# Optimization experiments

Hardware: AMD Instinct MI355X
Metric: run time of the kernel (lower is better)

## Reference

```python
import jax, jax.numpy as jnp
import numpy as np

IN_F = 4096
OUT_F = 4096
RANK = 16
TOKENS = 8192
WORDS = IN_F // 16  # 16 int2 codes per int32 word
LORA_SCALE = 1.0


def pack_int2(codes):
    """codes: [out_f, in_f] int32 in {0,1,2} -> packed [out_f, in_f//16] int32.
    Little-endian: code k of a word sits at bits [2k, 2k+1]."""
    c = codes.reshape(codes.shape[0], -1, 16)  # [out, words, 16]
    shifts = jnp.arange(16, dtype=jnp.int32) * 2
    return jnp.sum(c << shifts, axis=-1).astype(jnp.int32)


def unpack_int2(packed, in_features):
    """packed: [out_f, words] int32 -> ternary floats [out_f, in_f] in {-1,0,+1}."""
    shifts = jnp.arange(16, dtype=jnp.int32) * 2
    codes = (packed[:, :, None] >> shifts) & 3  # [out, words, 16]
    codes = codes.reshape(packed.shape[0], -1)[:, :in_features]
    return codes - 1  # {0,1,2} -> {-1,0,+1}


def setup_inputs() -> dict:
    key = jax.random.key(0)
    kx, kc, ka, km, kb, kA, kB = jax.random.split(key, 7)
    x = jax.random.normal(kx, (TOKENS, IN_F), dtype=jnp.float32)
    codes = jax.random.randint(kc, (OUT_F, IN_F), 0, 3, dtype=jnp.int32)  # {0,1,2}
    int2_packed = pack_int2(codes)  # [OUT_F, WORDS]
    alpha = jax.random.uniform(ka, (OUT_F,), dtype=jnp.float32) * 0.1 + 0.01
    mu = jax.random.normal(km, (OUT_F,), dtype=jnp.float32) * 0.01
    bias = jax.random.normal(kb, (OUT_F,), dtype=jnp.float32) * 0.02
    lora_A = jax.random.normal(kA, (RANK, IN_F), dtype=jnp.float32) * 0.02
    lora_B = jax.random.normal(kB, (OUT_F, RANK), dtype=jnp.float32) * 0.02
    return {"x": x, "int2_packed": int2_packed, "alpha": alpha, "mu": mu,
            "bias": bias, "lora_A": lora_A, "lora_B": lora_B}


def reference(x, int2_packed, alpha, mu, bias, lora_A, lora_B):
    # Unpack ternary weight T in {-1,0,+1}: [OUT_F, IN_F]
    T = unpack_int2(int2_packed, IN_F).astype(x.dtype)
    # ternary matmul, per-row scale alpha
    out = jnp.einsum('ti,oi->to', x, T) * alpha[None, :]
    # asymmetric shift: mu_o * sum_i x_i
    out = out + mu[None, :] * jnp.sum(x, axis=-1, keepdims=True)
    # LoRA correction: scale * (x A^T) B^T
    lora_out = jnp.einsum('tr,or->to', jnp.einsum('ti,ri->tr', x, lora_A), lora_B)
    out = out + LORA_SCALE * lora_out
    return out + bias[None, :]
```

## Files before the change

kernel.cpp:

```cpp
#include <hip/hip_runtime.h>
#include <stdint.h>

#define IN_F   4096
#define OUT_F  4096
#define TOKENS 8192
#define RANK   16

#define BM 128
#define BN 128
#define BKI 64

typedef unsigned short u16;
typedef __attribute__((ext_vector_type(8))) short bf16x8;
typedef __attribute__((ext_vector_type(4))) float f32x4;
typedef __attribute__((ext_vector_type(4))) int i32x4;

#define GLDS16(g, l) __builtin_amdgcn_global_load_lds( \
    (__attribute__((address_space(1))) void*)(g),      \
    (__attribute__((address_space(3))) void*)(l), 16, 0, 0)

__device__ __forceinline__ u16 bf16bits(float f) {
    unsigned int u = __builtin_bit_cast(unsigned int, f);
    unsigned int lsb = (u >> 16) & 1u;
    u += 0x7fffu + lsb;
    return (u16)(u >> 16);
}

__device__ __forceinline__ unsigned int quant4(float a, float b, float c, float d, float inv) {
    int qa = __float2int_rn(a * inv); qa = max(-127, min(127, qa));
    int qb = __float2int_rn(b * inv); qb = max(-127, min(127, qb));
    int qc = __float2int_rn(c * inv); qc = max(-127, min(127, qc));
    int qd = __float2int_rn(d * inv); qd = max(-127, min(127, qd));
    return (qa & 255) | ((qb & 255) << 8) | ((qc & 255) << 16) | ((qd & 255) << 24);
}

__global__ __launch_bounds__(256) void k_quant(const float* __restrict__ X,
                                               signed char* __restrict__ Xq,
                                               float* __restrict__ sArr,
                                               float* __restrict__ SArr) {
    const int t = blockIdx.x;
    const int tid = threadIdx.x;
    const int lane = tid & 63;
    const int wv = tid >> 6;

    const float4* X4 = (const float4*)(X + (size_t)t * IN_F);
    float4 v[4];
#pragma unroll
    for (int j = 0; j < 4; j++) v[j] = X4[tid * 4 + j];

    float s = 0.f, m = 0.f;
#pragma unroll
    for (int j = 0; j < 4; j++) {
        s += v[j].x + v[j].y + v[j].z + v[j].w;
        m = fmaxf(m, fmaxf(fmaxf(fabsf(v[j].x), fabsf(v[j].y)),
                           fmaxf(fabsf(v[j].z), fabsf(v[j].w))));
    }
#pragma unroll
    for (int off = 32; off > 0; off >>= 1) {
        s += __shfl_down(s, off);
        m = fmaxf(m, __shfl_down(m, off));
    }
    __shared__ float rs[4], rm[4];
    if (lane == 0) { rs[wv] = s; rm[wv] = m; }
    __syncthreads();
    float S = rs[0] + rs[1] + rs[2] + rs[3];
    float M = fmaxf(fmaxf(rm[0], rm[1]), fmaxf(rm[2], rm[3]));
    M = fmaxf(M, 1e-20f);
    if (tid == 0) { SArr[t] = S; sArr[t] = M / 127.0f; }

    float inv = 127.0f / M;
    uint4 o;
    o.x = quant4(v[0].x, v[0].y, v[0].z, v[0].w, inv);
    o.y = quant4(v[1].x, v[1].y, v[1].z, v[1].w, inv);
    o.z = quant4(v[2].x, v[2].y, v[2].z, v[2].w, inv);
    o.w = quant4(v[3].x, v[3].y, v[3].z, v[3].w, inv);
    *(uint4*)(Xq + (size_t)t * IN_F + tid * 16) = o;
}

__global__ __launch_bounds__(256) void k_aq(const float* __restrict__ lA,
                                            signed char* __restrict__ Aq,
                                            float* __restrict__ aScale) {
    const int r = blockIdx.x;
    const int tid = threadIdx.x;
    const int lane = tid & 63;
    const int wv = tid >> 6;

    const float4* A4 = (const float4*)(lA + (size_t)r * IN_F);
    float4 v[4];
#pragma unroll
    for (int j = 0; j < 4; j++) v[j] = A4[tid * 4 + j];

    float m = 0.f;
#pragma unroll
    for (int j = 0; j < 4; j++)
        m = fmaxf(m, fmaxf(fmaxf(fabsf(v[j].x), fabsf(v[j].y)),
                           fmaxf(fabsf(v[j].z), fabsf(v[j].w))));
#pragma unroll
    for (int off = 32; off > 0; off >>= 1) m = fmaxf(m, __shfl_down(m, off));
    __shared__ float rm[4];
    if (lane == 0) rm[wv] = m;
    __syncthreads();
    float M = fmaxf(fmaxf(rm[0], rm[1]), fmaxf(rm[2], rm[3]));
    M = fmaxf(M, 1e-20f);
    if (tid == 0) aScale[r] = M / 127.0f;

    float inv = 127.0f / M;
    uint4 o;
    o.x = quant4(v[0].x, v[0].y, v[0].z, v[0].w, inv);
    o.y = quant4(v[1].x, v[1].y, v[1].z, v[1].w, inv);
    o.z = quant4(v[2].x, v[2].y, v[2].z, v[2].w, inv);
    o.w = quant4(v[3].x, v[3].y, v[3].z, v[3].w, inv);
    *(uint4*)(Aq + (size_t)r * IN_F + tid * 16) = o;
}

__global__ __launch_bounds__(64) void k_lora_y(const signed char* __restrict__ Xq,
                                               const signed char* __restrict__ Aq,
                                               const float* __restrict__ sArr,
                                               const float* __restrict__ aScale,
                                               u16* __restrict__ ypad) {
    const int lane = threadIdx.x;
    const int t0 = blockIdx.x * 16;
    const int fr = lane & 15;
    const int q16 = (lane >> 4) * 16;

    i32x4 acc = {};
    const signed char* xrow = Xq + (size_t)(t0 + fr) * IN_F + q16;
    const signed char* arow = Aq + (size_t)fr * IN_F + q16;
#pragma unroll 8
    for (int k0 = 0; k0 < IN_F; k0 += BKI) {
        i32x4 af = *(const i32x4*)(xrow + k0);
        i32x4 bf = *(const i32x4*)(arow + k0);
        acc = __builtin_amdgcn_mfma_i32_16x16x64_i8(af, bf, acc, 0, 0, 0);
    }

    const int c0 = lane & 15;
    const int r0 = (lane >> 4) * 4;
    float asc = aScale[c0];
#pragma unroll
    for (int r = 0; r < 4; r++) {
        int t = t0 + r0 + r;
        float y = sArr[t] * asc * (float)acc[r];
        ypad[(size_t)t * 32 + c0] = bf16bits(y);
        ypad[(size_t)t * 32 + 16 + c0] = 0;
    }
}

__global__ __launch_bounds__(256) void k_build_wi8(const int* __restrict__ packed,
                                                   signed char* __restrict__ Wq) {
    int idx = blockIdx.x * 256 + threadIdx.x;
    int p = packed[idx];
    uint4 o;
    unsigned int w[4];
#pragma unroll
    for (int g = 0; g < 4; g++) {
        unsigned int word = 0;
#pragma unroll
        for (int j = 0; j < 4; j++) {
            int k = g * 4 + j;
            int b = ((p >> (2 * k)) & 3) - 1;
            word |= (unsigned int)(b & 255) << (8 * j);
        }
        w[g] = word;
    }
    o.x = w[0]; o.y = w[1]; o.z = w[2]; o.w = w[3];
    *(uint4*)(Wq + (size_t)idx * 16) = o;
}

__global__ __launch_bounds__(256) void k_bl(const float* __restrict__ lB,
                                            u16* __restrict__ Bl) {
    int o = blockIdx.x * 256 + threadIdx.x;
    const float4* B4 = (const float4*)(lB + (size_t)o * RANK);
    float4 b0 = B4[0], b1 = B4[1], b2 = B4[2], b3 = B4[3];
    union { u16 u[32]; uint4 q[4]; } ob;
    ob.u[0] = bf16bits(b0.x); ob.u[1] = bf16bits(b0.y); ob.u[2] = bf16bits(b0.z); ob.u[3] = bf16bits(b0.w);
    ob.u[4] = bf16bits(b1.x); ob.u[5] = bf16bits(b1.y); ob.u[6] = bf16bits(b1.z); ob.u[7] = bf16bits(b1.w);
    ob.u[8] = bf16bits(b2.x); ob.u[9] = bf16bits(b2.y); ob.u[10] = bf16bits(b2.z); ob.u[11] = bf16bits(b2.w);
    ob.u[12] = bf16bits(b3.x); ob.u[13] = bf16bits(b3.y); ob.u[14] = bf16bits(b3.z); ob.u[15] = bf16bits(b3.w);
#pragma unroll
    for (int k = 16; k < 32; k++) ob.u[k] = 0;
    uint4* dst = (uint4*)(Bl + (size_t)o * 32);
    dst[0] = ob.q[0]; dst[1] = ob.q[1]; dst[2] = ob.q[2]; dst[3] = ob.q[3];
}

__global__ __launch_bounds__(256, 2) void k_gemm_i8(const signed char* __restrict__ Xq,
                                                    const signed char* __restrict__ Wq,
                                                    const float* __restrict__ sArr,
                                                    const float* __restrict__ SArr,
                                                    const float* __restrict__ alpha,
                                                    const float* __restrict__ mu,
                                                    const float* __restrict__ bias,
                                                    const u16* __restrict__ ypad,
                                                    const u16* __restrict__ Bl,
                                                    float* __restrict__ out) {
    __shared__ unsigned char smem[16384];
    unsigned char* smA = smem;
    unsigned char* smB = smem + 8192;

    const int tid = threadIdx.x;
    const int lane = tid & 63;
    const int wv = tid >> 6;
    const int wm = (wv >> 1) * 64;
    const int wn = (wv & 1) * 64;
    const int fr = lane & 15;
    const int q16 = (lane >> 4) * 16;
    const int wvbase = wv * 1024;

    const int m0 = blockIdx.y * BM;
    const int n0 = blockIdx.x * BN;

    i32x4 acc[4][4] = {};

    for (int k0 = 0; k0 < IN_F; k0 += BKI) {
        __syncthreads();
#pragma unroll
        for (int i = 0; i < 2; i++) {
            int c = i * 256 + tid;
            int row = c >> 2, off = (c & 3) << 4;
            GLDS16(Xq + (size_t)(m0 + row) * IN_F + k0 + off, smA + i * 4096 + wvbase);
        }
#pragma unroll
        for (int i = 0; i < 2; i++) {
            int c = i * 256 + tid;
            int row = c >> 2, off = (c & 3) << 4;
            GLDS16(Wq + (size_t)(n0 + row) * IN_F + k0 + off, smB + i * 4096 + wvbase);
        }
        __syncthreads();

        i32x4 af[4], bf[4];
#pragma unroll
        for (int mt = 0; mt < 4; mt++)
            af[mt] = *(const i32x4*)(smA + (wm + mt * 16 + fr) * BKI + q16);
#pragma unroll
        for (int nt = 0; nt < 4; nt++)
            bf[nt] = *(const i32x4*)(smB + (wn + nt * 16 + fr) * BKI + q16);
#pragma unroll
        for (int mt = 0; mt < 4; mt++)
#pragma unroll
            for (int nt = 0; nt < 4; nt++)
                acc[mt][nt] = __builtin_amdgcn_mfma_i32_16x16x64_i8(af[mt], bf[nt], acc[mt][nt], 0, 0, 0);
    }

    const int r0 = (lane >> 4) * 4;
    const int c0 = lane & 15;
    f32x4 facc[4][4];
#pragma unroll
    for (int mt = 0; mt < 4; mt++) {
        int rb = m0 + wm + mt * 16 + r0;
        f32x4 sv = *(const f32x4*)(sArr + rb);
        f32x4 Sv = *(const f32x4*)(SArr + rb);
#pragma unroll
        for (int nt = 0; nt < 4; nt++) {
            int col = n0 + wn + nt * 16 + c0;
            float av = alpha[col], mv = mu[col], bv = bias[col];
#pragma unroll
            for (int r = 0; r < 4; r++)
                facc[mt][nt][r] = av * sv[r] * (float)acc[mt][nt][r] + fmaf(mv, Sv[r], bv);
        }
    }

    __syncthreads();
#pragma unroll
    for (int i = 0; i < 2; i++) {
        int c = i * 256 + tid;
        int row = c >> 2, off = (c & 3) << 4;
        GLDS16((const unsigned char*)ypad + (size_t)(m0 + row) * 64 + off, smA + i * 4096 + wvbase);
        GLDS16((const unsigned char*)Bl + (size_t)(n0 + row) * 64 + off, smB + i * 4096 + wvbase);
    }
    __syncthreads();
    bf16x8 yf[4], blf[4];
#pragma unroll
    for (int mt = 0; mt < 4; mt++)
        yf[mt] = *(const bf16x8*)(smA + (wm + mt * 16 + fr) * 64 + q16);
#pragma unroll
    for (int nt = 0; nt < 4; nt++)
        blf[nt] = *(const bf16x8*)(smB + (wn + nt * 16 + fr) * 64 + q16);
#pragma unroll
    for (int mt = 0; mt < 4; mt++)
#pragma unroll
        for (int nt = 0; nt < 4; nt++)
            facc[mt][nt] = __builtin_amdgcn_mfma_f32_16x16x32_bf16(yf[mt], blf[nt], facc[mt][nt], 0, 0, 0);

#pragma unroll
    for (int nt = 0; nt < 4; nt++) {
        int col = n0 + wn + nt * 16 + c0;
#pragma unroll
        for (int mt = 0; mt < 4; mt++) {
            int row = m0 + wm + mt * 16 + r0;
            float* op = out + (size_t)row * OUT_F + col;
#pragma unroll
            for (int r = 0; r < 4; r++)
                op[(size_t)r * OUT_F] = facc[mt][nt][r];
        }
    }
}

extern "C" void kernel_launch(void* const* d_in, const int* in_sizes, int n_in,
                              void* d_out, int out_size, void* d_ws, size_t ws_size,
                              hipStream_t stream) {
    const float* x      = (const float*)d_in[0];
    const int*   packed = (const int*)d_in[1];
    const float* alpha  = (const float*)d_in[2];
    const float* mu     = (const float*)d_in[3];
    const float* bias   = (const float*)d_in[4];
    const float* lA     = (const float*)d_in[5];
    const float* lB     = (const float*)d_in[6];
    float* out = (float*)d_out;

    char* p = (char*)d_ws;
    signed char* Wq = (signed char*)p;             p += (size_t)OUT_F * IN_F;
    signed char* Xq = (signed char*)p;             p += (size_t)TOKENS * IN_F;
    float* sArr = (float*)p;                       p += (size_t)TOKENS * 4;
    float* SArr = (float*)p;                       p += (size_t)TOKENS * 4;
    u16* ypad = (u16*)p;                           p += (size_t)TOKENS * 32 * 2;
    u16* Bl = (u16*)p;                             p += (size_t)OUT_F * 32 * 2;
    signed char* Aq = (signed char*)p;             p += (size_t)RANK * IN_F;
    float* aScale = (float*)p;                     p += RANK * 4;

    k_quant<<<dim3(TOKENS), dim3(256), 0, stream>>>(x, Xq, sArr, SArr);
    k_aq<<<dim3(RANK), dim3(256), 0, stream>>>(lA, Aq, aScale);
    k_lora_y<<<dim3(TOKENS / 16), dim3(64), 0, stream>>>(Xq, Aq, sArr, aScale, ypad);
    k_build_wi8<<<dim3(OUT_F * 256 / 256), dim3(256), 0, stream>>>(packed, Wq);
    k_bl<<<dim3(OUT_F / 256), dim3(256), 0, stream>>>(lB, Bl);

    dim3 grid(OUT_F / BN, TOKENS / BM);
    k_gemm_i8<<<grid, dim3(256), 0, stream>>>(Xq, Wq, sArr, SArr, alpha, mu, bias, ypad, Bl, out);
}
```

Measured before the change: 411.1 us.

## Fuse prep kernels, split-K LoRA projection, and swizzle GEMM LDS tiles

Merges the activation quantization, weight unpacking, LoRA-A quantization and LoRA-B conversion into one launch that dispatches on block index. The LoRA down-projection now uses four waves per block, each covering a quarter of K, with an LDS reduction. The main int8 GEMM XOR-swizzles the 16-byte chunks within each LDS row to cut bank conflicts on the fragment reads. This trades fewer launches and better LDS access for extra index arithmetic and block-type branching.

```diff
diff --git a/kernel.cpp b/kernel.cpp
--- a/kernel.cpp
+++ b/kernel.cpp
@@ -18,6 +18,10 @@
 #define GLDS16(g, l) __builtin_amdgcn_global_load_lds( \
     (__attribute__((address_space(1))) void*)(g),      \
     (__attribute__((address_space(3))) void*)(l), 16, 0, 0)
+
+__device__ __forceinline__ int swz_row(int row) {
+    return (row & 3) ^ ((row >> 2) & 1);
+}
 
 __device__ __forceinline__ u16 bf16bits(float f) {
     unsigned int u = __builtin_bit_cast(unsigned int, f);
@@ -34,152 +38,154 @@
     return (qa & 255) | ((qb & 255) << 8) | ((qc & 255) << 16) | ((qd & 255) << 24);
 }
 
-__global__ __launch_bounds__(256) void k_quant(const float* __restrict__ X,
-                                               signed char* __restrict__ Xq,
-                                               float* __restrict__ sArr,
-                                               float* __restrict__ SArr) {
-    const int t = blockIdx.x;
+__global__ __launch_bounds__(256) void k_prep(const float* __restrict__ X,
+                                              const int* __restrict__ packed,
+                                              const float* __restrict__ lA,
+                                              const float* __restrict__ lB,
+                                              signed char* __restrict__ Xq,
+                                              float* __restrict__ sArr,
+                                              float* __restrict__ SArr,
+                                              signed char* __restrict__ Wq,
+                                              u16* __restrict__ Bl,
+                                              signed char* __restrict__ Aq,
+                                              float* __restrict__ aScale) {
+    __shared__ float rs[4], rm[4];
+    const int b = blockIdx.x;
     const int tid = threadIdx.x;
     const int lane = tid & 63;
     const int wv = tid >> 6;
 
-    const float4* X4 = (const float4*)(X + (size_t)t * IN_F);
-    float4 v[4];
-#pragma unroll
-    for (int j = 0; j < 4; j++) v[j] = X4[tid * 4 + j];
-
-    float s = 0.f, m = 0.f;
-#pragma unroll
-    for (int j = 0; j < 4; j++) {
-        s += v[j].x + v[j].y + v[j].z + v[j].w;
-        m = fmaxf(m, fmaxf(fmaxf(fabsf(v[j].x), fabsf(v[j].y)),
-                           fmaxf(fabsf(v[j].z), fabsf(v[j].w))));
-    }
-#pragma unroll
-    for (int off = 32; off > 0; off >>= 1) {
-        s += __shfl_down(s, off);
-        m = fmaxf(m, __shfl_down(m, off));
-    }
-    __shared__ float rs[4], rm[4];
-    if (lane == 0) { rs[wv] = s; rm[wv] = m; }
-    __syncthreads();
-    float S = rs[0] + rs[1] + rs[2] + rs[3];
-    float M = fmaxf(fmaxf(rm[0], rm[1]), fmaxf(rm[2], rm[3]));
-    M = fmaxf(M, 1e-20f);
-    if (tid == 0) { SArr[t] = S; sArr[t] = M / 127.0f; }
-
-    float inv = 127.0f / M;
-    uint4 o;
-    o.x = quant4(v[0].x, v[0].y, v[0].z, v[0].w, inv);
-    o.y = quant4(v[1].x, v[1].y, v[1].z, v[1].w, inv);
-    o.z = quant4(v[2].x, v[2].y, v[2].z, v[2].w, inv);
-    o.w = quant4(v[3].x, v[3].y, v[3].z, v[3].w, inv);
-    *(uint4*)(Xq + (size_t)t * IN_F + tid * 16) = o;
-}
-
-__global__ __launch_bounds__(256) void k_aq(const float* __restrict__ lA,
-                                            signed char* __restrict__ Aq,
-                                            float* __restrict__ aScale) {
-    const int r = blockIdx.x;
+    if (b < TOKENS) {
+        const int t = b;
+        const float4* X4 = (const float4*)(X + (size_t)t * IN_F);
+        float4 v[4];
+#pragma unroll
+        for (int j = 0; j < 4; j++) v[j] = X4[tid * 4 + j];
+
+        float s = 0.f, m = 0.f;
+#pragma unroll
+        for (int j = 0; j < 4; j++) {
+            s += v[j].x + v[j].y + v[j].z + v[j].w;
+            m = fmaxf(m, fmaxf(fmaxf(fabsf(v[j].x), fabsf(v[j].y)),
+                               fmaxf(fabsf(v[j].z), fabsf(v[j].w))));
+        }
+#pragma unroll
+        for (int off = 32; off > 0; off >>= 1) {
+            s += __shfl_down(s, off);
+            m = fmaxf(m, __shfl_down(m, off));
+        }
+        if (lane == 0) { rs[wv] = s; rm[wv] = m; }
+        __syncthreads();
+        float S = rs[0] + rs[1] + rs[2] + rs[3];
+        float M = fmaxf(fmaxf(rm[0], rm[1]), fmaxf(rm[2], rm[3]));
+        M = fmaxf(M, 1e-20f);
+        if (tid == 0) { SArr[t] = S; sArr[t] = M / 127.0f; }
+
+        float inv = 127.0f / M;
+        uint4 o;
+        o.x = quant4(v[0].x, v[0].y, v[0].z, v[0].w, inv);
+        o.y = quant4(v[1].x, v[1].y, v[1].z, v[1].w, inv);
+        o.z = quant4(v[2].x, v[2].y, v[2].z, v[2].w, inv);
+        o.w = quant4(v[3].x, v[3].y, v[3].z, v[3].w, inv);
+        *(uint4*)(Xq + (size_t)t * IN_F + tid * 16) = o;
+    } else if (b < TOKENS + OUT_F * (IN_F / 16) / 256) {
+        int idx = (b - TOKENS) * 256 + tid;
+        int p = packed[idx];
+        uint4 o;
+        unsigned int w[4];
+#pragma unroll
+        for (int g = 0; g < 4; g++) {
+            unsigned int word = 0;
+#pragma unroll
+            for (int j = 0; j < 4; j++) {
+                int k = g * 4 + j;
+                int bb = ((p >> (2 * k)) & 3) - 1;
+                word |= (unsigned int)(bb & 255) << (8 * j);
+            }
+            w[g] = word;
+        }
+        o.x = w[0]; o.y = w[1]; o.z = w[2]; o.w = w[3];
+        *(uint4*)(Wq + (size_t)idx * 16) = o;
+    } else if (b < TOKENS + OUT_F * (IN_F / 16) / 256 + OUT_F / 256) {
+        int o = (b - TOKENS - OUT_F * (IN_F / 16) / 256) * 256 + tid;
+        const float4* B4 = (const float4*)(lB + (size_t)o * RANK);
+        float4 b0 = B4[0], b1 = B4[1], b2 = B4[2], b3 = B4[3];
+        union { u16 u[32]; uint4 q[4]; } ob;
+        ob.u[0] = bf16bits(b0.x); ob.u[1] = bf16bits(b0.y); ob.u[2] = bf16bits(b0.z); ob.u[3] = bf16bits(b0.w);
+        ob.u[4] = bf16bits(b1.x); ob.u[5] = bf16bits(b1.y); ob.u[6] = bf16bits(b1.z); ob.u[7] = bf16bits(b1.w);
+        ob.u[8] = bf16bits(b2.x); ob.u[9] = bf16bits(b2.y); ob.u[10] = bf16bits(b2.z); ob.u[11] = bf16bits(b2.w);
+        ob.u[12] = bf16bits(b3.x); ob.u[13] = bf16bits(b3.y); ob.u[14] = bf16bits(b3.z); ob.u[15] = bf16bits(b3.w);
+#pragma unroll
+        for (int k = 16; k < 32; k++) ob.u[k] = 0;
+        uint4* dst = (uint4*)(Bl + (size_t)o * 32);
+        dst[0] = ob.q[0]; dst[1] = ob.q[1]; dst[2] = ob.q[2]; dst[3] = ob.q[3];
+    } else {
+        const int r = b - (TOKENS + OUT_F * (IN_F / 16) / 256 + OUT_F / 256);
+        const float4* A4 = (const float4*)(lA + (size_t)r * IN_F);
+        float4 v[4];
+#pragma unroll
+        for (int j = 0; j < 4; j++) v[j] = A4[tid * 4 + j];
+
+        float m = 0.f;
+#pragma unroll
+        for (int j = 0; j < 4; j++)
+            m = fmaxf(m, fmaxf(fmaxf(fabsf(v[j].x), fabsf(v[j].y)),
+                               fmaxf(fabsf(v[j].z), fabsf(v[j].w))));
+#pragma unroll
+        for (int off = 32; off > 0; off >>= 1) m = fmaxf(m, __shfl_down(m, off));
+        if (lane == 0) rm[wv] = m;
+        __syncthreads();
+        float M = fmaxf(fmaxf(rm[0], rm[1]), fmaxf(rm[2], rm[3]));
+        M = fmaxf(M, 1e-20f);
+        if (tid == 0) aScale[r] = M / 127.0f;
+
+        float inv = 127.0f / M;
+        uint4 o;
+        o.x = quant4(v[0].x, v[0].y, v[0].z, v[0].w, inv);
+        o.y = quant4(v[1].x, v[1].y, v[1].z, v[1].w, inv);
+        o.z = quant4(v[2].x, v[2].y, v[2].z, v[2].w, inv);
+        o.w = quant4(v[3].x, v[3].y, v[3].z, v[3].w, inv);
+        *(uint4*)(Aq + (size_t)r * IN_F + tid * 16) = o;
+    }
+}
+
+__global__ __launch_bounds__(256) void k_lora_y(const signed char* __restrict__ Xq,
+                                                const signed char* __restrict__ Aq,
+                                                const float* __restrict__ sArr,
+                                                const float* __restrict__ aScale,
+                                                u16* __restrict__ ypad) {
+    __shared__ i32x4 red[4][64];
     const int tid = threadIdx.x;
     const int lane = tid & 63;
     const int wv = tid >> 6;
-
-    const float4* A4 = (const float4*)(lA + (size_t)r * IN_F);
-    float4 v[4];
-#pragma unroll
-    for (int j = 0; j < 4; j++) v[j] = A4[tid * 4 + j];
-
-    float m = 0.f;
-#pragma unroll
-    for (int j = 0; j < 4; j++)
-        m = fmaxf(m, fmaxf(fmaxf(fabsf(v[j].x), fabsf(v[j].y)),
-                           fmaxf(fabsf(v[j].z), fabsf(v[j].w))));
-#pragma unroll
-    for (int off = 32; off > 0; off >>= 1) m = fmaxf(m, __shfl_down(m, off));
-    __shared__ float rm[4];
-    if (lane == 0) rm[wv] = m;
-    __syncthreads();
-    float M = fmaxf(fmaxf(rm[0], rm[1]), fmaxf(rm[2], rm[3]));
-    M = fmaxf(M, 1e-20f);
-    if (tid == 0) aScale[r] = M / 127.0f;
-
-    float inv = 127.0f / M;
-    uint4 o;
-    o.x = quant4(v[0].x, v[0].y, v[0].z, v[0].w, inv);
-    o.y = quant4(v[1].x, v[1].y, v[1].z, v[1].w, inv);
-    o.z = quant4(v[2].x, v[2].y, v[2].z, v[2].w, inv);
-    o.w = quant4(v[3].x, v[3].y, v[3].z, v[3].w, inv);
-    *(uint4*)(Aq + (size_t)r * IN_F + tid * 16) = o;
-}
-
-__global__ __launch_bounds__(64) void k_lora_y(const signed char* __restrict__ Xq,
-                                               const signed char* __restrict__ Aq,
-                                               const float* __restrict__ sArr,
-                                               const float* __restrict__ aScale,
-                                               u16* __restrict__ ypad) {
-    const int lane = threadIdx.x;
     const int t0 = blockIdx.x * 16;
     const int fr = lane & 15;
     const int q16 = (lane >> 4) * 16;
 
     i32x4 acc = {};
-    const signed char* xrow = Xq + (size_t)(t0 + fr) * IN_F + q16;
-    const signed char* arow = Aq + (size_t)fr * IN_F + q16;
-#pragma unroll 8
-    for (int k0 = 0; k0 < IN_F; k0 += BKI) {
+    const signed char* xrow = Xq + (size_t)(t0 + fr) * IN_F + wv * 1024 + q16;
+    const signed char* arow = Aq + (size_t)fr * IN_F + wv * 1024 + q16;
+#pragma unroll
+    for (int k0 = 0; k0 < 1024; k0 += BKI) {
         i32x4 af = *(const i32x4*)(xrow + k0);
         i32x4 bf = *(const i32x4*)(arow + k0);
         acc = __builtin_amdgcn_mfma_i32_16x16x64_i8(af, bf, acc, 0, 0, 0);
     }
-
-    const int c0 = lane & 15;
-    const int r0 = (lane >> 4) * 4;
-    float asc = aScale[c0];
-#pragma unroll
-    for (int r = 0; r < 4; r++) {
-        int t = t0 + r0 + r;
-        float y = sArr[t] * asc * (float)acc[r];
-        ypad[(size_t)t * 32 + c0] = bf16bits(y);
-        ypad[(size_t)t * 32 + 16 + c0] = 0;
-    }
-}
-
-__global__ __launch_bounds__(256) void k_build_wi8(const int* __restrict__ packed,
-                                                   signed char* __restrict__ Wq) {
-    int idx = blockIdx.x * 256 + threadIdx.x;
-    int p = packed[idx];
-    uint4 o;
-    unsigned int w[4];
-#pragma unroll
-    for (int g = 0; g < 4; g++) {
-        unsigned int word = 0;
-#pragma unroll
-        for (int j = 0; j < 4; j++) {
-            int k = g * 4 + j;
-            int b = ((p >> (2 * k)) & 3) - 1;
-            word |= (unsigned int)(b & 255) << (8 * j);
-        }
-        w[g] = word;
-    }
-    o.x = w[0]; o.y = w[1]; o.z = w[2]; o.w = w[3];
-    *(uint4*)(Wq + (size_t)idx * 16) = o;
-}
-
-__global__ __launch_bounds__(256) void k_bl(const float* __restrict__ lB,
-                                            u16* __restrict__ Bl) {
-    int o = blockIdx.x * 256 + threadIdx.x;
-    const float4* B4 = (const float4*)(lB + (size_t)o * RANK);
-    float4 b0 = B4[0], b1 = B4[1], b2 = B4[2], b3 = B4[3];
-    union { u16 u[32]; uint4 q[4]; } ob;
-    ob.u[0] = bf16bits(b0.x); ob.u[1] = bf16bits(b0.y); ob.u[2] = bf16bits(b0.z); ob.u[3] = bf16bits(b0.w);
-    ob.u[4] = bf16bits(b1.x); ob.u[5] = bf16bits(b1.y); ob.u[6] = bf16bits(b1.z); ob.u[7] = bf16bits(b1.w);
-    ob.u[8] = bf16bits(b2.x); ob.u[9] = bf16bits(b2.y); ob.u[10] = bf16bits(b2.z); ob.u[11] = bf16bits(b2.w);
-    ob.u[12] = bf16bits(b3.x); ob.u[13] = bf16bits(b3.y); ob.u[14] = bf16bits(b3.z); ob.u[15] = bf16bits(b3.w);
-#pragma unroll
-    for (int k = 16; k < 32; k++) ob.u[k] = 0;
-    uint4* dst = (uint4*)(Bl + (size_t)o * 32);
-    dst[0] = ob.q[0]; dst[1] = ob.q[1]; dst[2] = ob.q[2]; dst[3] = ob.q[3];
+    red[wv][lane] = acc;
+    __syncthreads();
+    if (wv == 0) {
+        i32x4 s0 = red[0][lane], s1 = red[1][lane], s2 = red[2][lane], s3 = red[3][lane];
+        const int c0 = lane & 15;
+        const int r0 = (lane >> 4) * 4;
+        float asc = aScale[c0];
+#pragma unroll
+        for (int r = 0; r < 4; r++) {
+            int t = t0 + r0 + r;
+            float y = sArr[t] * asc * (float)(s0[r] + s1[r] + s2[r] + s3[r]);
+            ypad[(size_t)t * 32 + c0] = bf16bits(y);
+            ypad[(size_t)t * 32 + 16 + c0] = 0;
+        }
+    }
 }
 
 __global__ __launch_bounds__(256, 2) void k_gemm_i8(const signed char* __restrict__ Xq,
@@ -202,37 +208,41 @@
     const int wm = (wv >> 1) * 64;
     const int wn = (wv & 1) * 64;
     const int fr = lane & 15;
-    const int q16 = (lane >> 4) * 16;
+    const int qs = lane >> 4;
+    const int sw = swz_row(fr);
+    const int rdoff = ((qs ^ sw) << 4);
     const int wvbase = wv * 1024;
 
     const int m0 = blockIdx.y * BM;
     const int n0 = blockIdx.x * BN;
 
+    int srow[2], soff[2];
+#pragma unroll
+    for (int i = 0; i < 2; i++) {
+        int c = i * 256 + tid;
+        srow[i] = c >> 2;
+        soff[i] = (((c & 3) ^ swz_row(c >> 2)) << 4);
+    }
+
     i32x4 acc[4][4] = {};
 
     for (int k0 = 0; k0 < IN_F; k0 += BKI) {
         __syncthreads();
 #pragma unroll
-        for (int i = 0; i < 2; i++) {
-            int c = i * 256 + tid;
-            int row = c >> 2, off = (c & 3) << 4;
-            GLDS16(Xq + (size_t)(m0 + row) * IN_F + k0 + off, smA + i * 4096 + wvbase);
-        }
-#pragma unroll
-        for (int i = 0; i < 2; i++) {
-            int c = i * 256 + tid;
-            int row = c >> 2, off = (c & 3) << 4;
-            GLDS16(Wq + (size_t)(n0 + row) * IN_F + k0 + off, smB + i * 4096 + wvbase);
-        }
+        for (int i = 0; i < 2; i++)
+            GLDS16(Xq + (size_t)(m0 + srow[i]) * IN_F + k0 + soff[i], smA + i * 4096 + wvbase);
+#pragma unroll
+        for (int i = 0; i < 2; i++)
+            GLDS16(Wq + (size_t)(n0 + srow[i]) * IN_F + k0 + soff[i], smB + i * 4096 + wvbase);
         __syncthreads();
 
         i32x4 af[4], bf[4];
 #pragma unroll
         for (int mt = 0; mt < 4; mt++)
-            af[mt] = *(const i32x4*)(smA + (wm + mt * 16 + fr) * BKI + q16);
+            af[mt] = *(const i32x4*)(smA + (wm + mt * 16 + fr) * BKI + rdoff);
 #pragma unroll
         for (int nt = 0; nt < 4; nt++)
-            bf[nt] = *(const i32x4*)(smB + (wn + nt * 16 + fr) * BKI + q16);
+            bf[nt] = *(const i32x4*)(smB + (wn + nt * 16 + fr) * BKI + rdoff);
 #pragma unroll
         for (int mt = 0; mt < 4; mt++)
 #pragma unroll
@@ -261,19 +271,17 @@
     __syncthreads();
 #pragma unroll
     for (int i = 0; i < 2; i++) {
-        int c = i * 256 + tid;
-        int row = c >> 2, off = (c & 3) << 4;
-        GLDS16((const unsigned char*)ypad + (size_t)(m0 + row) * 64 + off, smA + i * 4096 + wvbase);
-        GLDS16((const unsigned char*)Bl + (size_t)(n0 + row) * 64 + off, smB + i * 4096 + wvbase);
+        GLDS16((const unsigned char*)ypad + (size_t)(m0 + srow[i]) * 64 + soff[i], smA + i * 4096 + wvbase);
+        GLDS16((const unsigned char*)Bl + (size_t)(n0 + srow[i]) * 64 + soff[i], smB + i * 4096 + wvbase);
     }
     __syncthreads();
     bf16x8 yf[4], blf[4];
 #pragma unroll
     for (int mt = 0; mt < 4; mt++)
-        yf[mt] = *(const bf16x8*)(smA + (wm + mt * 16 + fr) * 64 + q16);
+        yf[mt] = *(const bf16x8*)(smA + (wm + mt * 16 + fr) * 64 + rdoff);
 #pragma unroll
     for (int nt = 0; nt < 4; nt++)
-        blf[nt] = *(const bf16x8*)(smB + (wn + nt * 16 + fr) * 64 + q16);
+        blf[nt] = *(const bf16x8*)(smB + (wn + nt * 16 + fr) * 64 + rdoff);
 #pragma unroll
     for (int mt = 0; mt < 4; mt++)
 #pragma unroll
@@ -316,11 +324,9 @@
     signed char* Aq = (signed char*)p;             p += (size_t)RANK * IN_F;
     float* aScale = (float*)p;                     p += RANK * 4;
 
-    k_quant<<<dim3(TOKENS), dim3(256), 0, stream>>>(x, Xq, sArr, SArr);
-    k_aq<<<dim3(RANK), dim3(256), 0, stream>>>(lA, Aq, aScale);
-    k_lora_y<<<dim3(TOKENS / 16), dim3(64), 0, stream>>>(Xq, Aq, sArr, aScale, ypad);
-    k_build_wi8<<<dim3(OUT_F * 256 / 256), dim3(256), 0, stream>>>(packed, Wq);
-    k_bl<<<dim3(OUT_F / 256), dim3(256), 0, stream>>>(lB, Bl);
+    const int prep_blocks = TOKENS + OUT_F * (IN_F / 16) / 256 + OUT_F / 256 + RANK;
+    k_prep<<<dim3(prep_blocks), dim3(256), 0, stream>>>(x, packed, lA, lB, Xq, sArr, SArr, Wq, Bl, Aq, aScale);
+    k_lora_y<<<dim3(TOKENS / 16), dim3(256), 0, stream>>>(Xq, Aq, sArr, aScale, ypad);
 
     dim3 grid(OUT_F / BN, TOKENS / BM);
     k_gemm_i8<<<grid, dim3(256), 0, stream>>>(Xq, Wq, sArr, SArr, alpha, mu, bias, ypad, Bl, out);
```

Result: faster. 395.5 us (-3.8%).
